# Optimization experiments

Measured on AMD Instinct MI355X. Metric: run time of the kernel, lower is better.

## Reference

```python
import jax, jax.numpy as jnp
import numpy as np

D_IN = 768      # inp_dim
NH = 8          # head_num
HD = 96         # head_dim
HID = NH * HD   # 768
UP = 2 * D_IN   # p_factor[0]=2.0 -> 1536
FUSED = 2 * NH + 3 * HID  # 2320
KER = 4
CS = 64         # chunk_size
CAP = 15.0      # gate_soft_cap
EPS = 1e-6


def _ln(x, w, b):
    m = jnp.mean(x, -1, keepdims=True)
    v = jnp.mean((x - m) ** 2, -1, keepdims=True)
    return (x - m) / jnp.sqrt(v + EPS) * w + b


def setup_inputs() -> dict:
    key = jax.random.key(0)
    ks = jax.random.split(key, 10)
    B, S = 2, 4096
    def lin(k, fin, fout):
        return (jax.random.normal(k, (fin, fout), jnp.float32) / np.sqrt(fin)).astype(jnp.float32)
    return {
        "x": jax.random.normal(ks[0], (B, S, D_IN), jnp.float32),
        "ln_in_w": jnp.ones((D_IN,), jnp.float32), "ln_in_b": jnp.zeros((D_IN,), jnp.float32),
        "ln_hid_w": jnp.ones((HID,), jnp.float32), "ln_hid_b": jnp.zeros((HID,), jnp.float32),
        "up_l_w": lin(ks[1], D_IN, UP), "up_l_b": jnp.zeros((UP,), jnp.float32),
        "up_r_w": lin(ks[2], D_IN, HID), "up_r_b": jnp.zeros((HID,), jnp.float32),
        "down_w": lin(ks[3], HID, D_IN), "down_b": jnp.zeros((D_IN,), jnp.float32),
        "conv_w": (jax.random.normal(ks[4], (KER,), jnp.float32) * 0.5).astype(jnp.float32),
        "conv_b": jnp.zeros((), jnp.float32),
        "skip_w": lin(ks[5], UP, HID), "skip_b": jnp.zeros((HID,), jnp.float32),
        "fused_w": lin(ks[6], UP, FUSED), "fused_b": jnp.zeros((FUSED,), jnp.float32),
        "wo_w": lin(ks[7], UP, HID), "wo_b": jnp.zeros((HID,), jnp.float32),
    }


def reference(x, ln_in_w, ln_in_b, ln_hid_w, ln_hid_b, up_l_w, up_l_b, up_r_w, up_r_b,
              down_w, down_b, conv_w, conv_b, skip_w, skip_b, fused_w, fused_b, wo_w, wo_b):
    B, S, _ = x.shape
    soft_cap = lambda t: CAP * jnp.tanh(t / CAP)

    x_n = _ln(x, ln_in_w, ln_in_b)
    x_t = x_n @ up_l_w + up_l_b          # [B,S,UP]
    r_t = x_n @ up_r_w + up_r_b          # [B,S,HID]

    # causal conv: single shared (1,1,KER) kernel, depthwise across UP channels
    xp = jnp.pad(x_t, ((0, 0), (KER - 1, 0), (0, 0)))
    x_c = conv_b + sum(conv_w[j] * xp[:, j:j + S, :] for j in range(KER))
    x_c = jax.nn.silu(x_c)

    x_skip = x_c @ skip_w + skip_b
    proj = x_c @ fused_w + fused_b
    i_pre = soft_cap(proj[..., :NH])
    f_pre = soft_cap(proj[..., NH:2 * NH])
    q, k, v = jnp.split(proj[..., 2 * NH:], 3, axis=-1)
    o = jax.nn.sigmoid(x_t @ wo_w + wo_b)

    resh = lambda t: t.reshape(B, S, NH, HD).transpose(0, 2, 1, 3)  # [B,NH,S,HD]
    q = resh(q)
    k = resh(k) / np.sqrt(HD)
    v = resh(v)

    i_g = i_pre.transpose(0, 2, 1)  # [B,NH,S]
    f_g = f_pre.transpose(0, 2, 1)
    mx = jnp.maximum(f_g, i_g)
    i_g = jnp.exp(i_g - mx)
    f_g = jnp.exp(f_g - mx)

    NC = S // CS
    qc = q.reshape(B, NH, NC, CS, HD)
    kc = k.reshape(B, NH, NC, CS, HD)
    vc = v.reshape(B, NH, NC, CS, HD)
    ic = i_g.reshape(B, NH, NC, CS)
    fc = f_g.reshape(B, NH, NC, CS)

    lf = jnp.cumsum(jnp.log(fc + 1e-8), -1)          # [B,NH,NC,CS]
    f_cumul = jnp.exp(lf - lf[..., -1:])
    wC = f_cumul * ic
    # inter-chunk states; final_forget = exp(lf[-1]-lf[-1]) == 1 exactly -> exclusive cumsum
    C_contrib = jnp.einsum('bncl,bncld,bncle->bncde', wC, vc, kc)  # v-outer-k
    n_contrib = jnp.einsum('bncl,bncld->bncd', wC, kc)
    C_init = jnp.concatenate([jnp.zeros_like(C_contrib[:, :, :1]),
                              jnp.cumsum(C_contrib, axis=2)[:, :, :-1]], axis=2)
    n_init = jnp.concatenate([jnp.zeros_like(n_contrib[:, :, :1]),
                              jnp.cumsum(n_contrib, axis=2)[:, :, :-1]], axis=2)

    # intra-chunk, strictly-causal (j < i)
    mask = jnp.tril(jnp.ones((CS, CS), bool), -1)
    dl = lf[..., :, None] - lf[..., None, :]
    w = jnp.where(mask, ic[..., None, :] * jnp.exp(jnp.where(mask, dl, 0.0)), 0.0)
    scores = jnp.einsum('bncid,bncjd->bncij', qc, kc)
    attn = jax.nn.softmax(jnp.where(mask, scores, -1e30), axis=-1)
    attn = jnp.where(mask, attn, 0.0)  # pos 0 row -> all zeros

    h_intra = jnp.einsum('bncij,bncjd->bncid', attn * w, vc)
    n_intra = jnp.einsum('bncij,bncjd->bncid', w, kc)
    h_init = jnp.einsum('bncde,bncie->bncid', C_init, qc)

    total_n = n_init[..., None, :] + n_intra
    denom = jnp.maximum(jnp.sum(total_n * qc, -1, keepdims=True), 1.0)
    h = (h_init + h_intra) / denom                    # [B,NH,NC,CS,HD]

    h = h.reshape(B, NH, S, HD).transpose(0, 2, 1, 3).reshape(B, S, HID)
    h = o * h
    out = _ln(h, ln_hid_w, ln_hid_b) + x_skip
    out = out * jax.nn.silu(r_t)
    out = out @ down_w + down_b
    return out + x
```

## Files before the change

kernel.cpp:

```cpp
#include <hip/hip_runtime.h>
#include <hip/hip_bf16.h>
#include <math.h>

#define D_IN  768
#define NHD   8
#define HDIM  96
#define HID   768
#define UPD   1536
#define FUSED 2320
#define KER   4
#define CS    64
#define NCH   64
#define SB    4096
#define BB    2
#define NROW  (BB*SB)
#define NCHUNK (BB*NHD*NCH)
#define KSCALE 0.10206207261596577f

using u16   = unsigned short;
using frag8 = __attribute__((ext_vector_type(8))) short;
using f32x4 = __attribute__((ext_vector_type(4))) float;

#define O_WUPL   0
#define O_WUPR   1769472
#define O_WSKIP  2359296
#define O_WFUS   3538944
#define O_WWO    9142272
#define O_WDOWN  10321920
#define O_RT     10911744
#define O_XSKIP  17203200
#define O_LF     23494656
#define O_IC     23560192
#define O_WC     23625728
#define O_NC     23691264
#define O_XN     23789568
#define O_XT     33226752
#define O_XTS    45809664
#define O_PROJ   23789568
#define O_CC     45809664
#define O_H      55246848
#define O_OUT1   39518208

__device__ __forceinline__ void gld_lds16u(const u16* g, u16* l) {
    __builtin_amdgcn_global_load_lds(
        (const __attribute__((address_space(1))) void*)g,
        (__attribute__((address_space(3))) void*)l, 16, 0, 0);
}

__device__ __forceinline__ void split3u(float f, unsigned &H, unsigned &M, unsigned &L) {
    unsigned u = __float_as_uint(f);
    unsigned hr = (u + 0x7fffu + ((u >> 16) & 1u)) & 0xffff0000u;
    H = hr;
    float rm = f - __uint_as_float(hr);
    unsigned mr = __float_as_uint(rm) & 0xffff0000u;
    M = mr;
    float rl = rm - __uint_as_float(mr);
    L = __float_as_uint(rl) & 0xffff0000u;
}

__global__ __launch_bounds__(256) void tpose_split(
    const float* __restrict__ w, u16* __restrict__ tH, u16* __restrict__ tM,
    u16* __restrict__ tL, int K, int N)
{
    __shared__ float tile[64][65];
    int k0 = blockIdx.x * 64, n0 = blockIdx.y * 64;
    int t = threadIdx.x;
    int c = t & 63, r4 = t >> 6;
    #pragma unroll
    for (int it = 0; it < 16; ++it) {
        int r = r4 + it * 4;
        int n = n0 + c;
        tile[r][c] = (n < N) ? w[(size_t)(k0 + r) * N + n] : 0.f;
    }
    __syncthreads();
    #pragma unroll
    for (int it = 0; it < 16; ++it) {
        int nn = r4 + it * 4;
        float v = tile[c][nn];
        unsigned H, M, L;
        split3u(v, H, M, L);
        size_t idx = (size_t)(n0 + nn) * K + k0 + c;
        tH[idx] = (u16)(H >> 16);
        tM[idx] = (u16)(M >> 16);
        if (tL) tL[idx] = (u16)(L >> 16);
    }
}

__global__ __launch_bounds__(256) void ln_in_split(
    const float* __restrict__ x, const float* __restrict__ w,
    const float* __restrict__ b, u16* __restrict__ oH,
    u16* __restrict__ oM, u16* __restrict__ oL)
{
    int row = blockIdx.x;
    size_t base = (size_t)row * D_IN;
    int c0 = threadIdx.x, c1 = threadIdx.x + 256, c2 = threadIdx.x + 512;
    float v0 = x[base + c0], v1 = x[base + c1], v2 = x[base + c2];
    float s = v0 + v1 + v2;
    float ss = v0*v0 + v1*v1 + v2*v2;
    for (int off = 32; off; off >>= 1) { s += __shfl_xor(s, off); ss += __shfl_xor(ss, off); }
    __shared__ float red[8];
    int wid = threadIdx.x >> 6;
    if ((threadIdx.x & 63) == 0) { red[wid] = s; red[4 + wid] = ss; }
    __syncthreads();
    s = red[0] + red[1] + red[2] + red[3];
    ss = red[4] + red[5] + red[6] + red[7];
    float mean = s * (1.f / D_IN);
    float var = ss * (1.f / D_IN) - mean * mean;
    float inv = rsqrtf(var + 1e-6f);
    float r0 = (v0 - mean) * inv * w[c0] + b[c0];
    float r1 = (v1 - mean) * inv * w[c1] + b[c1];
    float r2 = (v2 - mean) * inv * w[c2] + b[c2];
    unsigned H, M, L;
    split3u(r0, H, M, L); oH[base+c0]=(u16)(H>>16); oM[base+c0]=(u16)(M>>16); oL[base+c0]=(u16)(L>>16);
    split3u(r1, H, M, L); oH[base+c1]=(u16)(H>>16); oM[base+c1]=(u16)(M>>16); oL[base+c1]=(u16)(L>>16);
    split3u(r2, H, M, L); oH[base+c2]=(u16)(H>>16); oM[base+c2]=(u16)(M>>16); oL[base+c2]=(u16)(L>>16);
}

template<int NT, int NTH>
__global__ __launch_bounds__(NTH) void gemm_sp(
    const u16* __restrict__ aH, const u16* __restrict__ aM, const u16* __restrict__ aL,
    const u16* __restrict__ bH, const u16* __restrict__ bM, const u16* __restrict__ bL,
    const float* __restrict__ bias, const float* __restrict__ resid,
    float* __restrict__ C, u16* __restrict__ cH, u16* __restrict__ cM,
    int N, int K, int act)
{
    constexpr int BM = (NT == 6) ? 256 : 128;
    __shared__ u16 AHM[2][BM * 64];
    __shared__ u16 BHM[2][128 * 64];
    __shared__ u16 ALp[(NT == 6) ? 2 : 1][(NT == 6) ? 128 * 64 : 8];
    __shared__ u16 BLp[(NT == 6) ? 2 : 1][(NT == 6) ? 64 * 64 : 8];

    int t = threadIdx.x;
    int wave = t >> 6, lane = t & 63;
    int lin = blockIdx.y * gridDim.x + blockIdx.x;
    int cpx = (gridDim.x * gridDim.y) >> 3;
    int sw  = (lin & 7) * cpx + (lin >> 3);
    int bx = sw % gridDim.x, by = sw / gridDim.x;
    int m0 = by * BM, n0 = bx * 128;

    int wm = (wave >> 1) * 64, wn = (wave & 1) * 64;
    f32x4 acc[4][4] = {};

    int l7 = lane & 7, l8 = lane >> 3;
    int lc = l7 ^ l8;
    int lane15 = lane & 15, rsel = lane >> 4;
    int pH = (rsel ^ l7) * 8;
    int pM = ((4 | rsel) ^ l7) * 8;
    int aLrow = (lane15 >> 1) * 64 + (((((lane & 1) << 2) | rsel) ^ (lane15 >> 1)) * 8);
    int wslot = wave;

    auto stage = [&](int buf, int k0) {
        if constexpr (NT == 6) {
            #pragma unroll
            for (int j = 0; j < 4; ++j) {
                int g = j * 8 + wslot;
                int r = g * 8 + l8;
                const u16* src = (lc >= 4 ? aM : aH) + (size_t)(m0 + r) * K + k0 + (lc & 3) * 8;
                gld_lds16u(src, &AHM[buf][g * 512 + lane * 8]);
            }
            #pragma unroll
            for (int j = 0; j < 2; ++j) {
                int g = j * 8 + wslot;
                int r = g * 8 + l8;
                const u16* src = (lc >= 4 ? bM : bH) + (size_t)(n0 + r) * K + k0 + (lc & 3) * 8;
                gld_lds16u(src, &BHM[buf][g * 512 + lane * 8]);
            }
            #pragma unroll
            for (int j = 0; j < 2; ++j) {
                int g = j * 8 + wslot;
                int R = g * 8 + l8;
                int rr = 2 * R + (lc >> 2);
                const u16* src = aL + (size_t)(m0 + rr) * K + k0 + (lc & 3) * 8;
                gld_lds16u(src, &ALp[buf][g * 512 + lane * 8]);
            }
            {
                int g = wslot;
                int R = g * 8 + l8;
                int rr = 2 * R + (lc >> 2);
                const u16* src = bL + (size_t)(n0 + rr) * K + k0 + (lc & 3) * 8;
                gld_lds16u(src, &BLp[buf][g * 512 + lane * 8]);
            }
        } else {
            #pragma unroll
            for (int j = 0; j < 4; ++j) {
                int g = j * 4 + wslot;
                int r = g * 8 + l8;
                const u16* src = (lc >= 4 ? aM : aH) + (size_t)(m0 + r) * K + k0 + (lc & 3) * 8;
                gld_lds16u(src, &AHM[buf][g * 512 + lane * 8]);
            }
            #pragma unroll
            for (int j = 0; j < 4; ++j) {
                int g = j * 4 + wslot;
                int r = g * 8 + l8;
                const u16* src = (lc >= 4 ? bM : bH) + (size_t)(n0 + r) * K + k0 + (lc & 3) * 8;
                gld_lds16u(src, &BHM[buf][g * 512 + lane * 8]);
            }
        }
    };

    auto compute = [&](int buf) {
        frag8 ah[4], am[4], al[(NT == 6) ? 4 : 1];
        #pragma unroll
        for (int mi = 0; mi < 4; ++mi) {
            int rr = wm + mi * 16 + lane15;
            const u16* bp = &AHM[buf][rr * 64];
            ah[mi] = *(const frag8*)&bp[pH];
            am[mi] = *(const frag8*)&bp[pM];
            if constexpr (NT == 6)
                al[mi] = *(const frag8*)&ALp[buf][(wm >> 1) * 64 + mi * 512 + aLrow];
        }
        #pragma unroll
        for (int ni = 0; ni < 4; ++ni) {
            int rb = wn + ni * 16 + lane15;
            const u16* bp = &BHM[buf][rb * 64];
            frag8 bh = *(const frag8*)&bp[pH];
            frag8 bm = *(const frag8*)&bp[pM];
            if constexpr (NT == 6) {
                frag8 bl = *(const frag8*)&BLp[buf][(wn >> 1) * 64 + ni * 512 + aLrow];
                #pragma unroll
                for (int mi = 0; mi < 4; ++mi) {
                    acc[mi][ni] = __builtin_amdgcn_mfma_f32_16x16x32_bf16(ah[mi], bm, acc[mi][ni], 0, 0, 0);
                    acc[mi][ni] = __builtin_amdgcn_mfma_f32_16x16x32_bf16(am[mi], bh, acc[mi][ni], 0, 0, 0);
                    acc[mi][ni] = __builtin_amdgcn_mfma_f32_16x16x32_bf16(ah[mi], bl, acc[mi][ni], 0, 0, 0);
                    acc[mi][ni] = __builtin_amdgcn_mfma_f32_16x16x32_bf16(al[mi], bh, acc[mi][ni], 0, 0, 0);
                    acc[mi][ni] = __builtin_amdgcn_mfma_f32_16x16x32_bf16(am[mi], bm, acc[mi][ni], 0, 0, 0);
                    acc[mi][ni] = __builtin_amdgcn_mfma_f32_16x16x32_bf16(ah[mi], bh, acc[mi][ni], 0, 0, 0);
                }
            } else {
                #pragma unroll
                for (int mi = 0; mi < 4; ++mi) {
                    acc[mi][ni] = __builtin_amdgcn_mfma_f32_16x16x32_bf16(ah[mi], bm, acc[mi][ni], 0, 0, 0);
                    acc[mi][ni] = __builtin_amdgcn_mfma_f32_16x16x32_bf16(am[mi], bh, acc[mi][ni], 0, 0, 0);
                    acc[mi][ni] = __builtin_amdgcn_mfma_f32_16x16x32_bf16(ah[mi], bh, acc[mi][ni], 0, 0, 0);
                }
            }
        }
    };

    int ns = K >> 5;
    stage(0, 0);
    asm volatile("" ::: "memory");
    int cur = 0;
    for (int s = 0; s < ns - 1; ++s) {
        stage(cur ^ 1, (s + 1) * 32);
        if constexpr (NT == 6) asm volatile("s_waitcnt vmcnt(9)" ::: "memory");
        else                   asm volatile("s_waitcnt vmcnt(8)" ::: "memory");
        __builtin_amdgcn_sched_barrier(0);
        __builtin_amdgcn_s_barrier();
        compute(cur);
        __builtin_amdgcn_s_barrier();
        cur ^= 1;
    }
    asm volatile("s_waitcnt vmcnt(0)" ::: "memory");
    __builtin_amdgcn_sched_barrier(0);
    __builtin_amdgcn_s_barrier();
    compute(cur);

    const bool dosplit = (cH != nullptr);
    #pragma unroll
    for (int ni = 0; ni < 4; ++ni) {
        int ncol = n0 + wn + ni * 16 + (lane & 15);
        if (ncol >= N) continue;
        float bs = bias[ncol];
        #pragma unroll
        for (int mi = 0; mi < 4; ++mi) {
            #pragma unroll
            for (int r = 0; r < 4; ++r) {
                int mrow = m0 + wm + mi * 16 + (lane >> 4) * 4 + r;
                float val = acc[mi][ni][r] + bs;
                if (act == 1) val = 1.f / (1.f + expf(-val));
                if (resid) val += resid[(size_t)mrow * N + ncol];
                C[(size_t)mrow * N + ncol] = val;
                if (dosplit) {
                    unsigned H, M, L;
                    split3u(val, H, M, L);
                    cH[(size_t)mrow * N + ncol] = (u16)(H >> 16);
                    cM[(size_t)mrow * N + ncol] = (u16)(M >> 16);
                }
            }
        }
    }
}

__global__ void conv_split(const float* __restrict__ xt, const float* __restrict__ cw,
                           const float* __restrict__ cb, u16* __restrict__ xcH,
                           u16* __restrict__ xcM, u16* __restrict__ xcL)
{
    size_t idx = (size_t)blockIdx.x * blockDim.x + threadIdx.x;
    if (idx >= (size_t)NROW * UPD) return;
    int ch = idx % UPD;
    int s = (int)((idx / UPD) % SB);
    int b = (int)(idx / ((size_t)UPD * SB));
    float acc = cb[0];
    #pragma unroll
    for (int j = 0; j < KER; ++j) {
        int sj = s - (KER - 1) + j;
        if (sj >= 0) acc += cw[j] * xt[((size_t)b * SB + sj) * UPD + ch];
    }
    float v = acc / (1.f + expf(-acc));
    unsigned H, M, L;
    split3u(v, H, M, L);
    xcH[idx] = (u16)(H >> 16);
    xcM[idx] = (u16)(M >> 16);
    xcL[idx] = (u16)(L >> 16);
}

__global__ __launch_bounds__(64) void gates_kernel(
    const float* __restrict__ proj, float* __restrict__ lf,
    float* __restrict__ ic, float* __restrict__ wC)
{
    int cid = blockIdx.x;
    int l = threadIdx.x;
    int b = cid >> 9;
    int nh = (cid >> 6) & 7;
    int c = cid & 63;
    int s = c * CS + l;
    size_t row = ((size_t)b * SB + s) * FUSED;
    float ip = proj[row + nh];
    float fp = proj[row + NHD + nh];
    ip = 15.f * tanhf(ip * (1.f / 15.f));
    fp = 15.f * tanhf(fp * (1.f / 15.f));
    float mx = fmaxf(ip, fp);
    float ig = expf(ip - mx);
    float fg = expf(fp - mx);
    float v = logf(fg + 1e-8f);
    for (int off = 1; off < 64; off <<= 1) {
        float u = __shfl_up(v, off);
        if (l >= off) v += u;
    }
    float last = __shfl(v, 63);
    lf[cid * CS + l] = v;
    ic[cid * CS + l] = ig;
    wC[cid * CS + l] = expf(v - last) * ig;
}

__global__ __launch_bounds__(256) void chunk_outer_kernel(
    const float* __restrict__ proj, const float* __restrict__ wC,
    float* __restrict__ Cc, float* __restrict__ nc)
{
    __shared__ float kL[CS * HDIM], vL[CS * HDIM], wL[CS];
    int cid = blockIdx.x, t = threadIdx.x;
    int b = cid >> 9, nh = (cid >> 6) & 7, c = cid & 63;
    const float* pg = proj + ((size_t)b * SB + (size_t)c * CS) * FUSED + 2 * NHD + nh * HDIM;
    for (int idx = t; idx < CS * HDIM; idx += 256) {
        int row = idx / HDIM, col = idx - row * HDIM;
        kL[idx] = pg[(size_t)row * FUSED + HID + col] * KSCALE;
        vL[idx] = pg[(size_t)row * FUSED + 2 * HID + col];
    }
    if (t < CS) wL[t] = wC[cid * CS + t];
    __syncthreads();
    int eb = t >> 3;
    int db = t & 7;
    float4 acc[3][3];
    #pragma unroll
    for (int e2 = 0; e2 < 3; ++e2)
        #pragma unroll
        for (int x = 0; x < 3; ++x) acc[e2][x] = make_float4(0.f, 0.f, 0.f, 0.f);
    for (int l = 0; l < CS; ++l) {
        float w = wL[l];
        float wk[3];
        #pragma unroll
        for (int e2 = 0; e2 < 3; ++e2) wk[e2] = w * kL[l * HDIM + 3 * eb + e2];
        const float* vr = &vL[l * HDIM + 12 * db];
        float4 vv[3];
        #pragma unroll
        for (int x = 0; x < 3; ++x) vv[x] = *(const float4*)(vr + 4 * x);
        #pragma unroll
        for (int e2 = 0; e2 < 3; ++e2)
            #pragma unroll
            for (int x = 0; x < 3; ++x) {
                acc[e2][x].x += wk[e2] * vv[x].x;
                acc[e2][x].y += wk[e2] * vv[x].y;
                acc[e2][x].z += wk[e2] * vv[x].z;
                acc[e2][x].w += wk[e2] * vv[x].w;
            }
    }
    float* Cb = Cc + (size_t)cid * HDIM * HDIM;
    #pragma unroll
    for (int e2 = 0; e2 < 3; ++e2)
        #pragma unroll
        for (int x = 0; x < 3; ++x)
            *(float4*)&Cb[(size_t)(3 * eb + e2) * HDIM + 12 * db + 4 * x] = acc[e2][x];
    if (t < HDIM) {
        float acc2 = 0.f;
        for (int l = 0; l < CS; ++l) acc2 += wL[l] * kL[l * HDIM + t];
        nc[(size_t)cid * HDIM + t] = acc2;
    }
}

__global__ void scan_kernel(float* __restrict__ Cc, float* __restrict__ nc)
{
    int gid = blockIdx.x * blockDim.x + threadIdx.x;
    const int NCE = BB * NHD * HDIM * HDIM;
    if (gid < NCE) {
        int bh = gid / (HDIM * HDIM);
        int ent = gid % (HDIM * HDIM);
        float run = 0.f;
        float* base = Cc + (size_t)bh * NCH * HDIM * HDIM + ent;
        for (int c = 0; c < NCH; ++c) {
            float tv = base[(size_t)c * HDIM * HDIM];
            base[(size_t)c * HDIM * HDIM] = run;
            run += tv;
        }
    } else {
        int g2 = gid - NCE;
        if (g2 < BB * NHD * HDIM) {
            int bh = g2 / HDIM, ent = g2 % HDIM;
            float run = 0.f;
            float* base = nc + (size_t)bh * NCH * HDIM + ent;
            for (int c = 0; c < NCH; ++c) {
                float tv = base[c * HDIM];
                base[c * HDIM] = run;
                run += tv;
            }
        }
    }
}

__global__ __launch_bounds__(256) void attn_kernel(
    const float* __restrict__ proj, const float* __restrict__ lf, const float* __restrict__ ic,
    const float* __restrict__ CiT, const float* __restrict__ ni,
    float* __restrict__ hout)
{
    __shared__ float qL[64 * 100];
    __shared__ float kL[64 * 100];
    __shared__ float lfL[64], icL[64], niL[96], dinvL[64];
    int cid = blockIdx.x, t = threadIdx.x;
    int b = cid >> 9, nh = (cid >> 6) & 7, c = cid & 63;
    const float* pq = proj + ((size_t)b * SB + (size_t)c * CS) * FUSED + 2 * NHD + nh * HDIM;
    const float* pk = pq + HID;
    const float* pv = pq + 2 * HID;
    #pragma unroll
    for (int it = 0; it < 6; ++it) {
        int idx = t + it * 256;
        int row = idx / 24, col = (idx % 24) * 4;
        *(float4*)&qL[row * 100 + col] = *(const float4*)(pq + (size_t)row * FUSED + col);
        float4 kv = *(const float4*)(pk + (size_t)row * FUSED + col);
        kv.x *= KSCALE; kv.y *= KSCALE; kv.z *= KSCALE; kv.w *= KSCALE;
        *(float4*)&kL[row * 100 + col] = kv;
    }
    if (t < 64) { lfL[t] = lf[cid * CS + t]; icL[t] = ic[cid * CS + t]; }
    else if (t < 160) { niL[t - 64] = ni[(size_t)cid * HDIM + (t - 64)]; }
    __syncthreads();

    int i = t >> 2, g = t & 3;
    const float* qrow = qL + i * 100;
    float sc[16];
    #pragma unroll
    for (int jj = 0; jj < 16; ++jj) sc[jj] = 0.f;
    for (int d4 = 0; d4 < 24; ++d4) {
        float4 qv = *(const float4*)(qrow + 4 * d4);
        #pragma unroll
        for (int jj = 0; jj < 16; ++jj) {
            float4 kv = *(const float4*)(kL + (g + 4 * jj) * 100 + 4 * d4);
            sc[jj] += qv.x * kv.x + qv.y * kv.y + qv.z * kv.z + qv.w * kv.w;
        }
    }
    float lfi = lfL[i];
    float wv[16];
    #pragma unroll
    for (int jj = 0; jj < 16; ++jj) {
        int j = g + 4 * jj;
        wv[jj] = (j < i) ? icL[j] * expf(lfi - lfL[j]) : 0.f;
    }
    float den = 0.f;
    #pragma unroll
    for (int jj = 0; jj < 16; ++jj) den += wv[jj] * sc[jj];
    #pragma unroll
    for (int dd = 0; dd < 24; ++dd) {
        int d = 24 * g + dd;
        den += niL[d] * qrow[d];
    }
    float m = -1e30f;
    #pragma unroll
    for (int jj = 0; jj < 16; ++jj) { int j = g + 4 * jj; if (j < i) m = fmaxf(m, sc[jj]); }
    m = fmaxf(m, __shfl_xor(m, 1)); m = fmaxf(m, __shfl_xor(m, 2));
    float p = 0.f;
    #pragma unroll
    for (int jj = 0; jj < 16; ++jj) {
        int j = g + 4 * jj;
        sc[jj] = (j < i) ? expf(sc[jj] - m) : 0.f;
        p += sc[jj];
    }
    p += __shfl_xor(p, 1); p += __shfl_xor(p, 2);
    float pinv = (p > 0.f) ? 1.f / p : 0.f;
    __syncthreads();
    float* awL = kL;
    #pragma unroll
    for (int jj = 0; jj < 16; ++jj) {
        int j = g + 4 * jj;
        awL[i * 68 + j] = sc[jj] * pinv * wv[jj];
    }
    den += __shfl_xor(den, 1); den += __shfl_xor(den, 2);
    if ((t & 3) == 0) dinvL[i] = 1.f / fmaxf(den, 1.f);
    __syncthreads();

    int i0 = (t >> 3) << 1, db = (t & 7) * 12;
    float4 h4[2][3];
    #pragma unroll
    for (int r = 0; r < 2; ++r)
        #pragma unroll
        for (int x = 0; x < 3; ++x) h4[r][x] = make_float4(0.f, 0.f, 0.f, 0.f);
    const float* vb = pv + db;
    const float* aw0 = awL + i0 * 68;
    for (int j = 0; j < 64; ++j) {
        float a0 = aw0[j];
        float a1 = aw0[68 + j];
        const float4* vr = (const float4*)(vb + (size_t)j * FUSED);
        #pragma unroll
        for (int x = 0; x < 3; ++x) {
            float4 vv = vr[x];
            h4[0][x].x += a0 * vv.x; h4[0][x].y += a0 * vv.y;
            h4[0][x].z += a0 * vv.z; h4[0][x].w += a0 * vv.w;
            h4[1][x].x += a1 * vv.x; h4[1][x].y += a1 * vv.y;
            h4[1][x].z += a1 * vv.z; h4[1][x].w += a1 * vv.w;
        }
    }
    const float* Cb = CiT + (size_t)cid * (HDIM * HDIM) + db;
    const float* qr0 = qL + i0 * 100;
    const float* qr1 = qr0 + 100;
    for (int e = 0; e < 96; ++e) {
        float q0 = qr0[e], q1 = qr1[e];
        const float4* cr = (const float4*)(Cb + e * HDIM);
        #pragma unroll
        for (int x = 0; x < 3; ++x) {
            float4 cv = cr[x];
            h4[0][x].x += q0 * cv.x; h4[0][x].y += q0 * cv.y;
            h4[0][x].z += q0 * cv.z; h4[0][x].w += q0 * cv.w;
            h4[1][x].x += q1 * cv.x; h4[1][x].y += q1 * cv.y;
            h4[1][x].z += q1 * cv.z; h4[1][x].w += q1 * cv.w;
        }
    }
    float di0 = dinvL[i0], di1 = dinvL[i0 + 1];
    int s0 = c * CS + i0;
    float4* hr0 = (float4*)(hout + (((size_t)b * SB + s0) * NHD + nh) * HDIM + db);
    float4* hr1 = (float4*)(hout + (((size_t)b * SB + s0 + 1) * NHD + nh) * HDIM + db);
    #pragma unroll
    for (int x = 0; x < 3; ++x) {
        float4 h0 = h4[0][x], h1 = h4[1][x];
        h0.x *= di0; h0.y *= di0; h0.z *= di0; h0.w *= di0;
        h1.x *= di1; h1.y *= di1; h1.z *= di1; h1.w *= di1;
        hr0[x] = h0;
        hr1[x] = h1;
    }
}

__global__ __launch_bounds__(256) void ln_hid_split(
    const float* __restrict__ h, const float* __restrict__ o,
    const float* __restrict__ xskip, const float* __restrict__ rt,
    const float* __restrict__ w, const float* __restrict__ bb,
    u16* __restrict__ oH, u16* __restrict__ oM)
{
    int row = blockIdx.x;
    size_t base = (size_t)row * HID;
    int c0 = threadIdx.x, c1 = threadIdx.x + 256, c2 = threadIdx.x + 512;
    float v0 = o[base + c0] * h[base + c0];
    float v1 = o[base + c1] * h[base + c1];
    float v2 = o[base + c2] * h[base + c2];
    float s = v0 + v1 + v2;
    float ss = v0*v0 + v1*v1 + v2*v2;
    for (int off = 32; off; off >>= 1) { s += __shfl_xor(s, off); ss += __shfl_xor(ss, off); }
    __shared__ float red[8];
    int wid = threadIdx.x >> 6;
    if ((threadIdx.x & 63) == 0) { red[wid] = s; red[4 + wid] = ss; }
    __syncthreads();
    s = red[0] + red[1] + red[2] + red[3];
    ss = red[4] + red[5] + red[6] + red[7];
    float mean = s * (1.f / HID);
    float var = ss * (1.f / HID) - mean * mean;
    float inv = rsqrtf(var + 1e-6f);
    float g0 = rt[base + c0], g1 = rt[base + c1], g2 = rt[base + c2];
    float r0 = ((v0 - mean) * inv * w[c0] + bb[c0] + xskip[base + c0]) * (g0 / (1.f + expf(-g0)));
    float r1 = ((v1 - mean) * inv * w[c1] + bb[c1] + xskip[base + c1]) * (g1 / (1.f + expf(-g1)));
    float r2 = ((v2 - mean) * inv * w[c2] + bb[c2] + xskip[base + c2]) * (g2 / (1.f + expf(-g2)));
    unsigned H, M, L;
    split3u(r0, H, M, L); oH[base+c0]=(u16)(H>>16); oM[base+c0]=(u16)(M>>16);
    split3u(r1, H, M, L); oH[base+c1]=(u16)(H>>16); oM[base+c1]=(u16)(M>>16);
    split3u(r2, H, M, L); oH[base+c2]=(u16)(H>>16); oM[base+c2]=(u16)(M>>16);
}

extern "C" void kernel_launch(void* const* d_in, const int* in_sizes, int n_in,
                              void* d_out, int out_size, void* d_ws, size_t ws_size,
                              hipStream_t stream)
{
    const float* x       = (const float*)d_in[0];
    const float* ln_in_w = (const float*)d_in[1];
    const float* ln_in_b = (const float*)d_in[2];
    const float* ln_hid_w= (const float*)d_in[3];
    const float* ln_hid_b= (const float*)d_in[4];
    const float* up_l_w  = (const float*)d_in[5];
    const float* up_l_b  = (const float*)d_in[6];
    const float* up_r_w  = (const float*)d_in[7];
    const float* up_r_b  = (const float*)d_in[8];
    const float* down_w  = (const float*)d_in[9];
    const float* down_b  = (const float*)d_in[10];
    const float* conv_w  = (const float*)d_in[11];
    const float* conv_b  = (const float*)d_in[12];
    const float* skip_w  = (const float*)d_in[13];
    const float* skip_b  = (const float*)d_in[14];
    const float* fused_w = (const float*)d_in[15];
    const float* fused_b = (const float*)d_in[16];
    const float* wo_w    = (const float*)d_in[17];
    const float* wo_b    = (const float*)d_in[18];
    float* out = (float*)d_out;

    float* ws = (float*)d_ws;
    u16* wuplH = (u16*)(ws + O_WUPL);  u16* wuplM = wuplH + 1179648; u16* wuplL = wuplM + 1179648;
    u16* wuprH = (u16*)(ws + O_WUPR);  u16* wuprM = wuprH + 589824;
    u16* wskpH = (u16*)(ws + O_WSKIP); u16* wskpM = wskpH + 1179648;
    u16* wfusH = (u16*)(ws + O_WFUS);  u16* wfusM = wfusH + 3735552; u16* wfusL = wfusM + 3735552;
    u16* wwoH  = (u16*)(ws + O_WWO);   u16* wwoM  = wwoH  + 1179648;
    u16* wdwnH = (u16*)(ws + O_WDOWN); u16* wdwnM = wdwnH + 589824;
    float* rt    = ws + O_RT;
    float* xskip = ws + O_XSKIP;
    float* lf    = ws + O_LF;
    float* ic    = ws + O_IC;
    float* wC    = ws + O_WC;
    float* nc    = ws + O_NC;
    u16* xnH = (u16*)(ws + O_XN);  u16* xnM = xnH + 6291456; u16* xnL = xnM + 6291456;
    float* xt = ws + O_XT;
    u16* xtH = (u16*)(ws + O_XTS); u16* xtM = xtH + 12582912;
    u16* xcH = (u16*)(ws + O_XTS); u16* xcM = xcH + 12582912; u16* xcL = xcM + 12582912;
    float* proj = ws + O_PROJ;
    float* Cc = ws + O_CC;
    float* h  = ws + O_H;
    u16* out1H = (u16*)(ws + O_OUT1); u16* out1M = out1H + 6291456;
    float* o = (float*)d_out;

    tpose_split<<<dim3(12, 24), 256, 0, stream>>>(up_l_w, wuplH, wuplM, wuplL, 768, 1536);
    tpose_split<<<dim3(12, 12), 256, 0, stream>>>(up_r_w, wuprH, wuprM, nullptr, 768, 768);
    tpose_split<<<dim3(24, 12), 256, 0, stream>>>(skip_w, wskpH, wskpM, nullptr, 1536, 768);
    tpose_split<<<dim3(24, 38), 256, 0, stream>>>(fused_w, wfusH, wfusM, wfusL, 1536, 2320);
    tpose_split<<<dim3(24, 12), 256, 0, stream>>>(wo_w, wwoH, wwoM, nullptr, 1536, 768);
    tpose_split<<<dim3(12, 12), 256, 0, stream>>>(down_w, wdwnH, wdwnM, nullptr, 768, 768);
    ln_in_split<<<NROW, 256, 0, stream>>>(x, ln_in_w, ln_in_b, xnH, xnM, xnL);
    gemm_sp<6,512><<<dim3(12, 32), 512, 0, stream>>>(xnH, xnM, xnL, wuplH, wuplM, wuplL,
        up_l_b, nullptr, xt, xtH, xtM, UPD, D_IN, 0);
    gemm_sp<3,256><<<dim3(6, 64), 256, 0, stream>>>(xnH, xnM, nullptr, wuprH, wuprM, nullptr,
        up_r_b, nullptr, rt, nullptr, nullptr, HID, D_IN, 0);
    gemm_sp<3,256><<<dim3(6, 64), 256, 0, stream>>>(xtH, xtM, nullptr, wwoH, wwoM, nullptr,
        wo_b, nullptr, o, nullptr, nullptr, HID, UPD, 1);
    {
        size_t tot = (size_t)NROW * UPD;
        conv_split<<<(unsigned)((tot + 255) / 256), 256, 0, stream>>>(xt, conv_w, conv_b, xcH, xcM, xcL);
    }
    gemm_sp<3,256><<<dim3(6, 64), 256, 0, stream>>>(xcH, xcM, nullptr, wskpH, wskpM, nullptr,
        skip_b, nullptr, xskip, nullptr, nullptr, HID, UPD, 0);
    gemm_sp<6,512><<<dim3(19, 32), 512, 0, stream>>>(xcH, xcM, xcL, wfusH, wfusM, wfusL,
        fused_b, nullptr, proj, nullptr, nullptr, FUSED, UPD, 0);
    gates_kernel<<<NCHUNK, 64, 0, stream>>>(proj, lf, ic, wC);
    chunk_outer_kernel<<<NCHUNK, 256, 0, stream>>>(proj, wC, Cc, nc);
    {
        int tot = BB * NHD * HDIM * HDIM + BB * NHD * HDIM;
        scan_kernel<<<(tot + 255) / 256, 256, 0, stream>>>(Cc, nc);
    }
    attn_kernel<<<NCHUNK, 256, 0, stream>>>(proj, lf, ic, Cc, nc, h);
    ln_hid_split<<<NROW, 256, 0, stream>>>(h, o, xskip, rt, ln_hid_w, ln_hid_b, out1H, out1M);
    gemm_sp<3,256><<<dim3(6, 64), 256, 0, stream>>>(out1H, out1M, nullptr, wdwnH, wdwnM, nullptr,
        down_b, x, out, nullptr, nullptr, D_IN, HID, 0);
}
```

Before: 1.119 ms.

## Fold up_l and wo projections into one weight, merge with up_r GEMM

Precomputes W' = up_l_w @ wo_w and a folded bias so the output gate o is computed straight from x_n with K=768 instead of from x_t with K=1536. That GEMM is merged into the up_r GEMM as a second N-range writing to a second output, so the up_l GEMM no longer needs to emit split x_t copies. It also stages v into LDS in the attention kernel. The cost is extra per-call weight-prep kernels (a 768x768x1536 GEMM and a bias reduction) and small rounding differences from the refactored product.

```diff
diff --git a/kernel.cpp b/kernel.cpp
--- a/kernel.cpp
+++ b/kernel.cpp
@@ -40,6 +40,9 @@
 #define O_CC     45809664
 #define O_H      55246848
 #define O_OUT1   39518208
+#define A_UPLW   (O_XN)
+#define A_WWO3   (O_XN + 1769472)
+#define A_WP     (O_XN + 3538944)
 
 __device__ __forceinline__ void gld_lds16u(const u16* g, u16* l) {
     __builtin_amdgcn_global_load_lds(
@@ -84,6 +87,30 @@
         tM[idx] = (u16)(M >> 16);
         if (tL) tL[idx] = (u16)(L >> 16);
     }
+}
+
+__global__ __launch_bounds__(256) void split_noT(
+    const float* __restrict__ w, u16* __restrict__ tH, u16* __restrict__ tM,
+    u16* __restrict__ tL, int total)
+{
+    int idx = blockIdx.x * 256 + threadIdx.x;
+    if (idx >= total) return;
+    unsigned H, M, L;
+    split3u(w[idx], H, M, L);
+    tH[idx] = (u16)(H >> 16);
+    tM[idx] = (u16)(M >> 16);
+    tL[idx] = (u16)(L >> 16);
+}
+
+__global__ __launch_bounds__(256) void bias_fold(
+    const float* __restrict__ upb, const float* __restrict__ wow,
+    const float* __restrict__ wob, float* __restrict__ bp)
+{
+    int h = blockIdx.x * 256 + threadIdx.x;
+    float acc = wob[h];
+    #pragma unroll 8
+    for (int u = 0; u < UPD; ++u) acc += upb[u] * wow[(size_t)u * HID + h];
+    bp[h] = acc;
 }
 
 __global__ __launch_bounds__(256) void ln_in_split(
@@ -122,7 +149,9 @@
     const u16* __restrict__ bH, const u16* __restrict__ bM, const u16* __restrict__ bL,
     const float* __restrict__ bias, const float* __restrict__ resid,
     float* __restrict__ C, u16* __restrict__ cH, u16* __restrict__ cM,
-    int N, int K, int act)
+    int ldC, int N, int K, int act,
+    const u16* __restrict__ b2H, const u16* __restrict__ b2M, int bN1,
+    float* __restrict__ C2, const float* __restrict__ bias2, int act2)
 {
     constexpr int BM = (NT == 6) ? 256 : 128;
     __shared__ u16 AHM[2][BM * 64];
@@ -132,11 +161,18 @@
 
     int t = threadIdx.x;
     int wave = t >> 6, lane = t & 63;
-    int lin = blockIdx.y * gridDim.x + blockIdx.x;
-    int cpx = (gridDim.x * gridDim.y) >> 3;
-    int sw  = (lin & 7) * cpx + (lin >> 3);
-    int bx = sw % gridDim.x, by = sw / gridDim.x;
+    int tot = gridDim.x * gridDim.y;
+    int bx, by;
+    if ((tot & 7) == 0) {
+        int lin = blockIdx.y * gridDim.x + blockIdx.x;
+        int cpx = tot >> 3;
+        int sw  = (lin & 7) * cpx + (lin >> 3);
+        bx = sw % gridDim.x; by = sw / gridDim.x;
+    } else { bx = blockIdx.x; by = blockIdx.y; }
     int m0 = by * BM, n0 = bx * 128;
+
+    const u16* bHu = bH; const u16* bMu = bM; int nb = n0;
+    if (b2H != nullptr && n0 >= bN1) { bHu = b2H; bMu = b2M; nb = n0 - bN1; }
 
     int wm = (wave >> 1) * 64, wn = (wave & 1) * 64;
     f32x4 acc[4][4] = {};
@@ -162,7 +198,7 @@
             for (int j = 0; j < 2; ++j) {
                 int g = j * 8 + wslot;
                 int r = g * 8 + l8;
-                const u16* src = (lc >= 4 ? bM : bH) + (size_t)(n0 + r) * K + k0 + (lc & 3) * 8;
+                const u16* src = (lc >= 4 ? bMu : bHu) + (size_t)(nb + r) * K + k0 + (lc & 3) * 8;
                 gld_lds16u(src, &BHM[buf][g * 512 + lane * 8]);
             }
             #pragma unroll
@@ -177,7 +213,7 @@
                 int g = wslot;
                 int R = g * 8 + l8;
                 int rr = 2 * R + (lc >> 2);
-                const u16* src = bL + (size_t)(n0 + rr) * K + k0 + (lc & 3) * 8;
+                const u16* src = bL + (size_t)(nb + rr) * K + k0 + (lc & 3) * 8;
                 gld_lds16u(src, &BLp[buf][g * 512 + lane * 8]);
             }
         } else {
@@ -192,7 +228,7 @@
             for (int j = 0; j < 4; ++j) {
                 int g = j * 4 + wslot;
                 int r = g * 8 + l8;
-                const u16* src = (lc >= 4 ? bM : bH) + (size_t)(n0 + r) * K + k0 + (lc & 3) * 8;
+                const u16* src = (lc >= 4 ? bMu : bHu) + (size_t)(nb + r) * K + k0 + (lc & 3) * 8;
                 gld_lds16u(src, &BHM[buf][g * 512 + lane * 8]);
             }
         }
@@ -261,21 +297,26 @@
     for (int ni = 0; ni < 4; ++ni) {
         int ncol = n0 + wn + ni * 16 + (lane & 15);
         if (ncol >= N) continue;
-        float bs = bias[ncol];
+        bool r2 = (C2 != nullptr) && (ncol >= bN1);
+        float* Cp = r2 ? C2 : C;
+        int ld = r2 ? 768 : ldC;
+        int cc = r2 ? ncol - bN1 : ncol;
+        float bs = r2 ? (bias2 ? bias2[cc] : 0.f) : (bias ? bias[ncol] : 0.f);
+        int aa = r2 ? act2 : act;
         #pragma unroll
         for (int mi = 0; mi < 4; ++mi) {
             #pragma unroll
             for (int r = 0; r < 4; ++r) {
                 int mrow = m0 + wm + mi * 16 + (lane >> 4) * 4 + r;
                 float val = acc[mi][ni][r] + bs;
-                if (act == 1) val = 1.f / (1.f + expf(-val));
-                if (resid) val += resid[(size_t)mrow * N + ncol];
-                C[(size_t)mrow * N + ncol] = val;
-                if (dosplit) {
+                if (aa == 1) val = 1.f / (1.f + expf(-val));
+                if (resid && !r2) val += resid[(size_t)mrow * ld + cc];
+                Cp[(size_t)mrow * ld + cc] = val;
+                if (dosplit && !r2) {
                     unsigned H, M, L;
                     split3u(val, H, M, L);
-                    cH[(size_t)mrow * N + ncol] = (u16)(H >> 16);
-                    cM[(size_t)mrow * N + ncol] = (u16)(M >> 16);
+                    cH[(size_t)mrow * ld + cc] = (u16)(H >> 16);
+                    cM[(size_t)mrow * ld + cc] = (u16)(M >> 16);
                 }
             }
         }
@@ -424,6 +465,7 @@
 {
     __shared__ float qL[64 * 100];
     __shared__ float kL[64 * 100];
+    __shared__ float vL[64 * 100];
     __shared__ float lfL[64], icL[64], niL[96], dinvL[64];
     int cid = blockIdx.x, t = threadIdx.x;
     int b = cid >> 9, nh = (cid >> 6) & 7, c = cid & 63;
@@ -438,6 +480,7 @@
         float4 kv = *(const float4*)(pk + (size_t)row * FUSED + col);
         kv.x *= KSCALE; kv.y *= KSCALE; kv.z *= KSCALE; kv.w *= KSCALE;
         *(float4*)&kL[row * 100 + col] = kv;
+        *(float4*)&vL[row * 100 + col] = *(const float4*)(pv + (size_t)row * FUSED + col);
     }
     if (t < 64) { lfL[t] = lf[cid * CS + t]; icL[t] = ic[cid * CS + t]; }
     else if (t < 160) { niL[t - 64] = ni[(size_t)cid * HDIM + (t - 64)]; }
@@ -501,12 +544,12 @@
     for (int r = 0; r < 2; ++r)
         #pragma unroll
         for (int x = 0; x < 3; ++x) h4[r][x] = make_float4(0.f, 0.f, 0.f, 0.f);
-    const float* vb = pv + db;
+    const float* vb = vL + db;
     const float* aw0 = awL + i0 * 68;
     for (int j = 0; j < 64; ++j) {
         float a0 = aw0[j];
         float a1 = aw0[68 + j];
-        const float4* vr = (const float4*)(vb + (size_t)j * FUSED);
+        const float4* vr = (const float4*)(vb + j * 100);
         #pragma unroll
         for (int x = 0; x < 3; ++x) {
             float4 vv = vr[x];
@@ -609,7 +652,8 @@
     u16* wuprH = (u16*)(ws + O_WUPR);  u16* wuprM = wuprH + 589824;
     u16* wskpH = (u16*)(ws + O_WSKIP); u16* wskpM = wskpH + 1179648;
     u16* wfusH = (u16*)(ws + O_WFUS);  u16* wfusM = wfusH + 3735552; u16* wfusL = wfusM + 3735552;
-    u16* wwoH  = (u16*)(ws + O_WWO);   u16* wwoM  = wwoH  + 1179648;
+    u16* WtH   = (u16*)(ws + O_WWO);   u16* WtM   = WtH + 589824;
+    float* bprime = ws + O_WWO + 589824;
     u16* wdwnH = (u16*)(ws + O_WDOWN); u16* wdwnM = wdwnH + 589824;
     float* rt    = ws + O_RT;
     float* xskip = ws + O_XSKIP;
@@ -617,9 +661,11 @@
     float* ic    = ws + O_IC;
     float* wC    = ws + O_WC;
     float* nc    = ws + O_NC;
+    u16* uplwH = (u16*)(ws + A_UPLW); u16* uplwM = uplwH + 1179648; u16* uplwL = uplwM + 1179648;
+    u16* wwo3H = (u16*)(ws + A_WWO3); u16* wwo3M = wwo3H + 1179648; u16* wwo3L = wwo3M + 1179648;
+    float* Wp = ws + A_WP;
     u16* xnH = (u16*)(ws + O_XN);  u16* xnM = xnH + 6291456; u16* xnL = xnM + 6291456;
     float* xt = ws + O_XT;
-    u16* xtH = (u16*)(ws + O_XTS); u16* xtM = xtH + 12582912;
     u16* xcH = (u16*)(ws + O_XTS); u16* xcM = xcH + 12582912; u16* xcL = xcM + 12582912;
     float* proj = ws + O_PROJ;
     float* Cc = ws + O_CC;
@@ -627,27 +673,35 @@
     u16* out1H = (u16*)(ws + O_OUT1); u16* out1M = out1H + 6291456;
     float* o = (float*)d_out;
 
+    split_noT<<<4608, 256, 0, stream>>>(up_l_w, uplwH, uplwM, uplwL, 768 * 1536);
+    tpose_split<<<dim3(24, 12), 256, 0, stream>>>(wo_w, wwo3H, wwo3M, wwo3L, 1536, 768);
+    gemm_sp<6,512><<<dim3(6, 3), 512, 0, stream>>>(uplwH, uplwM, uplwL, wwo3H, wwo3M, wwo3L,
+        nullptr, nullptr, Wp, nullptr, nullptr, 768, 768, 1536, 0,
+        nullptr, nullptr, 1 << 30, nullptr, nullptr, 0);
+    bias_fold<<<3, 256, 0, stream>>>(up_l_b, wo_w, wo_b, bprime);
+    tpose_split<<<dim3(12, 12), 256, 0, stream>>>(Wp, WtH, WtM, nullptr, 768, 768);
     tpose_split<<<dim3(12, 24), 256, 0, stream>>>(up_l_w, wuplH, wuplM, wuplL, 768, 1536);
     tpose_split<<<dim3(12, 12), 256, 0, stream>>>(up_r_w, wuprH, wuprM, nullptr, 768, 768);
     tpose_split<<<dim3(24, 12), 256, 0, stream>>>(skip_w, wskpH, wskpM, nullptr, 1536, 768);
     tpose_split<<<dim3(24, 38), 256, 0, stream>>>(fused_w, wfusH, wfusM, wfusL, 1536, 2320);
-    tpose_split<<<dim3(24, 12), 256, 0, stream>>>(wo_w, wwoH, wwoM, nullptr, 1536, 768);
     tpose_split<<<dim3(12, 12), 256, 0, stream>>>(down_w, wdwnH, wdwnM, nullptr, 768, 768);
     ln_in_split<<<NROW, 256, 0, stream>>>(x, ln_in_w, ln_in_b, xnH, xnM, xnL);
     gemm_sp<6,512><<<dim3(12, 32), 512, 0, stream>>>(xnH, xnM, xnL, wuplH, wuplM, wuplL,
-        up_l_b, nullptr, xt, xtH, xtM, UPD, D_IN, 0);
-    gemm_sp<3,256><<<dim3(6, 64), 256, 0, stream>>>(xnH, xnM, nullptr, wuprH, wuprM, nullptr,
-        up_r_b, nullptr, rt, nullptr, nullptr, HID, D_IN, 0);
-    gemm_sp<3,256><<<dim3(6, 64), 256, 0, stream>>>(xtH, xtM, nullptr, wwoH, wwoM, nullptr,
-        wo_b, nullptr, o, nullptr, nullptr, HID, UPD, 1);
+        up_l_b, nullptr, xt, nullptr, nullptr, UPD, UPD, D_IN, 0,
+        nullptr, nullptr, 1 << 30, nullptr, nullptr, 0);
+    gemm_sp<3,256><<<dim3(12, 64), 256, 0, stream>>>(xnH, xnM, nullptr, wuprH, wuprM, nullptr,
+        up_r_b, nullptr, rt, nullptr, nullptr, 768, 1536, D_IN, 0,
+        WtH, WtM, 768, o, bprime, 1);
     {
         size_t tot = (size_t)NROW * UPD;
         conv_split<<<(unsigned)((tot + 255) / 256), 256, 0, stream>>>(xt, conv_w, conv_b, xcH, xcM, xcL);
     }
     gemm_sp<3,256><<<dim3(6, 64), 256, 0, stream>>>(xcH, xcM, nullptr, wskpH, wskpM, nullptr,
-        skip_b, nullptr, xskip, nullptr, nullptr, HID, UPD, 0);
+        skip_b, nullptr, xskip, nullptr, nullptr, HID, HID, UPD, 0,
+        nullptr, nullptr, 1 << 30, nullptr, nullptr, 0);
     gemm_sp<6,512><<<dim3(19, 32), 512, 0, stream>>>(xcH, xcM, xcL, wfusH, wfusM, wfusL,
-        fused_b, nullptr, proj, nullptr, nullptr, FUSED, UPD, 0);
+        fused_b, nullptr, proj, nullptr, nullptr, FUSED, FUSED, UPD, 0,
+        nullptr, nullptr, 1 << 30, nullptr, nullptr, 0);
     gates_kernel<<<NCHUNK, 64, 0, stream>>>(proj, lf, ic, wC);
     chunk_outer_kernel<<<NCHUNK, 256, 0, stream>>>(proj, wC, Cc, nc);
     {
@@ -657,5 +711,6 @@
     attn_kernel<<<NCHUNK, 256, 0, stream>>>(proj, lf, ic, Cc, nc, h);
     ln_hid_split<<<NROW, 256, 0, stream>>>(h, o, xskip, rt, ln_hid_w, ln_hid_b, out1H, out1M);
     gemm_sp<3,256><<<dim3(6, 64), 256, 0, stream>>>(out1H, out1M, nullptr, wdwnH, wdwnM, nullptr,
-        down_b, x, out, nullptr, nullptr, D_IN, HID, 0);
-}
+        down_b, x, out, nullptr, nullptr, D_IN, D_IN, HID, 0,
+        nullptr, nullptr, 1 << 30, nullptr, nullptr, 0);
+}
```

Result: slower. 1.272 ms (+13.8%).
